# Kernel tuning notes

Measured on AMD Instinct MI355X. Metric: run time of the kernel, lower is better.

Reference implementation:

```python
import jax, jax.numpy as jnp
import numpy as np

N_QUBITS = 20
W_MUL = (2.0 ** 0.5) * (5.0 ** -0.5)  # he_std = gain * 5**-0.5, use_wscale=True, lrmul=1

_C = jnp.complex64
X = jnp.array([[0, 1], [1, 0]], dtype=_C)
Y = jnp.array([[0, -1j], [1j, 0]], dtype=_C)
Z = jnp.array([[1, 0], [0, -1]], dtype=_C)
I2 = jnp.eye(2, dtype=_C)
I4 = jnp.eye(4, dtype=_C)
XX = jnp.kron(X, X)
YY = jnp.kron(Y, Y)
ZZ = jnp.kron(Z, Z)


def _rot(theta, pauli, ident):
    # exp(-i * theta/2 * P) = cos(theta/2) I - i sin(theta/2) P
    a = theta * 0.5
    return jnp.cos(a) * ident - (1j * jnp.sin(a)) * pauli


def _apply_1q(state, g, w):
    # state: [batch] + [2]*n ; contract gate input index with qubit axis w
    s = jnp.tensordot(g, state, axes=((1,), (w + 1,)))
    return jnp.moveaxis(s, 0, w + 1)


def _apply_2q(state, g4, w0, w1):
    g = g4.reshape(2, 2, 2, 2)  # (out0, out1, in0, in1)
    s = jnp.tensordot(g, state, axes=((2, 3), (w0 + 1, w1 + 1)))
    return jnp.moveaxis(s, (0, 1), (w0 + 1, w1 + 1))


def _xyz_layer(psi, params, n):
    # params: [3n]; rx, ry, rz on each wire
    for q in range(n):
        psi = _apply_1q(psi, _rot(params[3 * q], X, I2), q)
        psi = _apply_1q(psi, _rot(params[3 * q + 1], Y, I2), q)
        psi = _apply_1q(psi, _rot(params[3 * q + 2], Z, I2), q)
    return psi


def _circuit(psi, w, n):
    psi = _xyz_layer(psi, w[: 3 * n], n)
    for q in range(n - 1):
        i = 3 * n + 3 * q
        psi = _apply_2q(psi, _rot(w[i], XX, I4), q, q + 1)
        psi = _apply_2q(psi, _rot(w[i + 1], YY, I4), q, q + 1)
        psi = _apply_2q(psi, _rot(w[i + 2], ZZ, I4), q, q + 1)
    psi = _xyz_layer(psi, w[6 * n - 3 :], n)
    return psi


def setup_inputs() -> dict:
    key = jax.random.key(0)
    k1, k2 = jax.random.split(key)
    n = N_QUBITS
    dim = 1 << n
    batch = 4
    x = jax.random.normal(k1, (batch, 1, dim), dtype=jnp.float32)
    weight = jax.random.uniform(k2, (9 * n - 3,), dtype=jnp.float32, minval=0.0, maxval=2.0 * np.pi)
    return {"x": x, "weight": weight, "dimA": 10}


def reference(x, weight, dimA):
    n = N_QUBITS
    batch = x.shape[0]
    w = weight * W_MUL
    psi = x.astype(_C).reshape((batch,) + (2,) * n)  # MPS tensor [b, 2, ..., 2]
    psi = _circuit(psi, w, n)
    dimB = n - dimA
    # partial trace of |psi><psi| over the first dimB qubits (most-significant axes):
    # reduced[a, c] = sum_t psi[t, a] * conj(psi[t, c])  -- never materialize the full DM
    psi = psi.reshape(batch, 1 << dimB, 1 << dimA)
    rdm = jnp.einsum('bta,btc->bac', psi, psi.conj())
    # return real/imag stacked on last axis (real-valued representation of complex DM)
    return jnp.stack([rdm.real, rdm.imag], axis=-1)
```

## Files before the change

### kernel.cpp

```cpp
#include <hip/hip_runtime.h>
#include <hip/hip_bf16.h>

#define N_Q    20
#define DIM    (1 << N_Q)
#define BATCH  4
#define NGATES 19
#define L2OFF  117

typedef float2 c32;
typedef __attribute__((ext_vector_type(8))) short short8;
typedef __attribute__((ext_vector_type(4))) float f32x4;

__device__ __forceinline__ c32 cmul(c32 a, c32 b) {
    return make_float2(fmaf(a.x, b.x, -a.y * b.y), fmaf(a.x, b.y, a.y * b.x));
}
__device__ __forceinline__ c32 cmadd(c32 acc, c32 a, c32 b) {
    acc.x = fmaf(a.x, b.x, fmaf(-a.y, b.y, acc.x));
    acc.y = fmaf(a.x, b.y, fmaf(a.y, b.x, acc.y));
    return acc;
}
__device__ __forceinline__ unsigned short f2bf(float f) {
    union { float f; unsigned u; } v; v.f = f;
    unsigned r = v.u + 0x7FFFu + ((v.u >> 16) & 1u);
    return (unsigned short)(r >> 16);
}

__device__ void mm2(const c32 A[2][2], const c32 B[2][2], c32 C[2][2]) {
    for (int i = 0; i < 2; i++)
        for (int j = 0; j < 2; j++) {
            c32 s = make_float2(0.f, 0.f);
            for (int k = 0; k < 2; k++) s = cmadd(s, A[i][k], B[k][j]);
            C[i][j] = s;
        }
}
__device__ void mm4(const c32 A[4][4], const c32 B[4][4], c32 C[4][4]) {
    for (int i = 0; i < 4; i++)
        for (int j = 0; j < 4; j++) {
            c32 s = make_float2(0.f, 0.f);
            for (int k = 0; k < 4; k++) s = cmadd(s, A[i][k], B[k][j]);
            C[i][j] = s;
        }
}
__device__ void single_u(const float* w, int base, c32 U[2][2]) {
    const float WM = 0.63245553203367586640f;
    float hx = w[base] * WM * 0.5f, hy = w[base + 1] * WM * 0.5f, hz = w[base + 2] * WM * 0.5f;
    float cx = cosf(hx), sx = sinf(hx);
    float cy = cosf(hy), sy = sinf(hy);
    float cz = cosf(hz), sz = sinf(hz);
    c32 RX[2][2] = {{{cx, 0.f}, {0.f, -sx}}, {{0.f, -sx}, {cx, 0.f}}};
    c32 RY[2][2] = {{{cy, 0.f}, {-sy, 0.f}}, {{sy, 0.f}, {cy, 0.f}}};
    c32 RZ[2][2] = {{{cz, -sz}, {0.f, 0.f}}, {{0.f, 0.f}, {cz, sz}}};
    c32 T[2][2];
    mm2(RY, RX, T);
    mm2(RZ, T, U);
}
__device__ void kron22(const c32 A[2][2], const c32 B[2][2], c32 K[4][4]) {
    for (int i = 0; i < 2; i++)
        for (int j = 0; j < 2; j++)
            for (int k = 0; k < 2; k++)
                for (int l = 0; l < 2; l++)
                    K[i * 2 + j][k * 2 + l] = cmul(A[i][k], B[j][l]);
}

__global__ void build_gates(const float* __restrict__ w, c32* __restrict__ G) {
    int q = threadIdx.x;
    if (q >= NGATES) return;
    const float WM = 0.63245553203367586640f;
    float hx = w[60 + 3 * q] * WM * 0.5f;
    float hy = w[61 + 3 * q] * WM * 0.5f;
    float hz = w[62 + 3 * q] * WM * 0.5f;
    float cx = cosf(hx), sx = sinf(hx);
    float cy = cosf(hy), sy = sinf(hy);
    float cz = cosf(hz), sz = sinf(hz);
    c32 RXX[4][4], RYY[4][4], RZZ[4][4];
    for (int i = 0; i < 4; i++)
        for (int j = 0; j < 4; j++) {
            RXX[i][j] = make_float2(0.f, 0.f);
            RYY[i][j] = make_float2(0.f, 0.f);
            RZZ[i][j] = make_float2(0.f, 0.f);
        }
    for (int i = 0; i < 4; i++) {
        RXX[i][i]     = make_float2(cx, 0.f);
        RXX[i][3 - i] = make_float2(0.f, -sx);
        RYY[i][i]     = make_float2(cy, 0.f);
    }
    RYY[0][3] = make_float2(0.f,  sy);
    RYY[1][2] = make_float2(0.f, -sy);
    RYY[2][1] = make_float2(0.f, -sy);
    RYY[3][0] = make_float2(0.f,  sy);
    RZZ[0][0] = make_float2(cz, -sz);
    RZZ[1][1] = make_float2(cz,  sz);
    RZZ[2][2] = make_float2(cz,  sz);
    RZZ[3][3] = make_float2(cz, -sz);
    c32 T[4][4], M[4][4];
    mm4(RYY, RXX, T);
    mm4(RZZ, T, M);

    c32 I2m[2][2] = {{{1.f, 0.f}, {0.f, 0.f}}, {{0.f, 0.f}, {1.f, 0.f}}};
    c32 Ua[2][2], Ub[2][2], Pre[4][4], Post[4][4];
    if (q == 0) {
        single_u(w, 0, Ua);
        single_u(w, 3, Ub);
        kron22(Ua, Ub, Pre);
    } else {
        single_u(w, 3 * (q + 1), Ub);
        kron22(I2m, Ub, Pre);
    }
    if (q == NGATES - 1) {
        single_u(w, L2OFF + 3 * 18, Ua);
        single_u(w, L2OFF + 3 * 19, Ub);
        kron22(Ua, Ub, Post);
    } else {
        single_u(w, L2OFF + 3 * q, Ua);
        kron22(Ua, I2m, Post);
    }
    c32 T2[4][4], Gq[4][4];
    mm4(M, Pre, T2);
    mm4(Post, T2, Gq);
    for (int i = 0; i < 4; i++)
        for (int j = 0; j < 4; j++)
            G[q * 16 + i * 4 + j] = Gq[i][j];
}

__device__ __forceinline__ void apply4(const c32* g, c32& x0, c32& x1, c32& x2, c32& x3) {
    c32 r0 = cmul(g[0],  x0); r0 = cmadd(r0, g[1],  x1); r0 = cmadd(r0, g[2],  x2); r0 = cmadd(r0, g[3],  x3);
    c32 r1 = cmul(g[4],  x0); r1 = cmadd(r1, g[5],  x1); r1 = cmadd(r1, g[6],  x2); r1 = cmadd(r1, g[7],  x3);
    c32 r2 = cmul(g[8],  x0); r2 = cmadd(r2, g[9],  x1); r2 = cmadd(r2, g[10], x2); r2 = cmadd(r2, g[11], x3);
    c32 r3 = cmul(g[12], x0); r3 = cmadd(r3, g[13], x1); r3 = cmadd(r3, g[14], x2); r3 = cmadd(r3, g[15], x3);
    x0 = r0; x1 = r1; x2 = r2; x3 = r3;
}
__device__ __forceinline__ void load_gate(const c32* __restrict__ gp, c32 g[16]) {
#pragma unroll
    for (int k = 0; k < 16; k++) g[k] = gp[k];
}
template <int LO>
__device__ __forceinline__ void gate_on32(c32 v[32], const c32 g[16]) {
#pragma unroll
    for (int m = 0; m < 8; ++m) {
        const int j0 = ((m >> LO) << (LO + 2)) | (m & ((1 << LO) - 1));
        const int s = 1 << LO;
        apply4(g, v[j0], v[j0 + s], v[j0 + 2 * s], v[j0 + 3 * s]);
    }
}
template <int LO>
__device__ __forceinline__ void gate_on16(c32* v, const c32 g[16]) {
#pragma unroll
    for (int m = 0; m < 4; ++m) {
        const int j0 = ((m >> LO) << (LO + 2)) | (m & ((1 << LO) - 1));
        const int s = 1 << LO;
        apply4(g, v[j0], v[j0 + s], v[j0 + 2 * s], v[j0 + 3 * s]);
    }
}

#define SIDX(l) ((l) ^ ((((l) >> 5) & 15)))

__global__ __launch_bounds__(256) void pass_a2(const float* __restrict__ x,
                                               c32* __restrict__ psi,
                                               const c32* __restrict__ Gall) {
    __shared__ c32 s[8192];
    int b = blockIdx.x >> 7;
    int c0 = (blockIdx.x & 127) << 5;
    const float* xp = x + ((size_t)b << 20) + c0;
    c32* pp = psi + ((size_t)b << 20) + c0;
    int t = threadIdx.x;
    int col = t & 31, rlow = t >> 5;
    c32 v[32], g[16];
#pragma unroll
    for (int j = 0; j < 32; ++j) {
        int row = (j << 3) | rlow;
        v[j] = make_float2(xp[(size_t)row * 4096 + col], 0.f);
    }
    load_gate(Gall + 0 * 16, g);  gate_on32<3>(v, g);
    load_gate(Gall + 1 * 16, g);  gate_on32<2>(v, g);
    load_gate(Gall + 2 * 16, g);  gate_on32<1>(v, g);
    load_gate(Gall + 3 * 16, g);  gate_on32<0>(v, g);
#pragma unroll
    for (int j = 0; j < 32; ++j) {
        int l = ((((j << 3) | rlow) << 5)) | col;
        s[SIDX(l)] = v[j];
    }
    __syncthreads();
    int rhi = t >> 5;
#pragma unroll
    for (int rtop = 0; rtop < 2; ++rtop)
#pragma unroll
        for (int j = 0; j < 16; ++j) {
            int row = (rtop << 7) | (rhi << 4) | j;
            int l = (row << 5) | col;
            v[rtop * 16 + j] = s[SIDX(l)];
        }
    load_gate(Gall + 4 * 16, g);  gate_on16<2>(v, g);  gate_on16<2>(v + 16, g);
    load_gate(Gall + 5 * 16, g);  gate_on16<1>(v, g);  gate_on16<1>(v + 16, g);
    load_gate(Gall + 6 * 16, g);  gate_on16<0>(v, g);  gate_on16<0>(v + 16, g);
#pragma unroll
    for (int rtop = 0; rtop < 2; ++rtop)
#pragma unroll
        for (int j = 0; j < 16; ++j) {
            int row = (rtop << 7) | (rhi << 4) | j;
            pp[(size_t)row * 4096 + col] = v[rtop * 16 + j];
        }
}

__global__ __launch_bounds__(256) void pass_b2(const c32* __restrict__ psi,
                                               unsigned short* __restrict__ Brt,
                                               unsigned short* __restrict__ Bit,
                                               const c32* __restrict__ Gall) {
    __shared__ c32 s[8192];
    int b = blockIdx.x >> 7;
    int chunk = blockIdx.x & 127;
    const c32* pp = psi + ((size_t)b << 20) + ((size_t)chunk << 13);
    int t = threadIdx.x;
    c32 v[32], g[16];
#pragma unroll
    for (int j = 0; j < 32; ++j) v[j] = pp[(j << 8) | t];
    load_gate(Gall + 7 * 16, g);   gate_on32<3>(v, g);
    load_gate(Gall + 8 * 16, g);   gate_on32<2>(v, g);
    load_gate(Gall + 9 * 16, g);   gate_on32<1>(v, g);
    load_gate(Gall + 10 * 16, g);  gate_on32<0>(v, g);
#pragma unroll
    for (int j = 0; j < 32; ++j) { int l = (j << 8) | t; s[SIDX(l)] = v[j]; }
    __syncthreads();
    int hi2 = (t >> 4) << 9, lo2 = t & 15;
#pragma unroll
    for (int j = 0; j < 32; ++j) { int l = hi2 | (j << 4) | lo2; v[j] = s[SIDX(l)]; }
    load_gate(Gall + 11 * 16, g);  gate_on32<3>(v, g);
    load_gate(Gall + 12 * 16, g);  gate_on32<2>(v, g);
    load_gate(Gall + 13 * 16, g);  gate_on32<1>(v, g);
    load_gate(Gall + 14 * 16, g);  gate_on32<0>(v, g);
    __syncthreads();
#pragma unroll
    for (int j = 0; j < 32; ++j) { int l = hi2 | (j << 4) | lo2; s[SIDX(l)] = v[j]; }
    __syncthreads();
#pragma unroll
    for (int j = 0; j < 32; ++j) { int l = (t << 5) | j; v[j] = s[SIDX(l)]; }
    load_gate(Gall + 15 * 16, g);  gate_on32<3>(v, g);
    load_gate(Gall + 16 * 16, g);  gate_on32<2>(v, g);
    load_gate(Gall + 17 * 16, g);  gate_on32<1>(v, g);
    load_gate(Gall + 18 * 16, g);  gate_on32<0>(v, g);
    size_t off = ((size_t)b << 20) + ((size_t)chunk << 13) + ((size_t)t << 5);
#pragma unroll
    for (int p = 0; p < 4; ++p) {
        unsigned short rr[8], ri[8];
#pragma unroll
        for (int i = 0; i < 8; ++i) {
            rr[i] = f2bf(v[8 * p + i].x);
            ri[i] = f2bf(v[8 * p + i].y);
        }
        *reinterpret_cast<float4*>(Brt + off + 8 * p) = *reinterpret_cast<float4*>(rr);
        *reinterpret_cast<float4*>(Bit + off + 8 * p) = *reinterpret_cast<float4*>(ri);
    }
}

__global__ __launch_bounds__(256) void bt_t(const unsigned short* __restrict__ Brt,
                                            const unsigned short* __restrict__ Bit,
                                            unsigned short* __restrict__ Art,
                                            unsigned short* __restrict__ Ait) {
    __shared__ unsigned lds32[64 * 66];
    int b  = blockIdx.z;
    int t0 = blockIdx.x * 64;
    int a0 = blockIdx.y * 64;
    size_t gb = (size_t)b << 20;
#pragma unroll
    for (int h = 0; h < 2; ++h) {
        int p = threadIdx.x + h * 256;
        int r = p >> 3, cq = p & 7;
        size_t src = gb + (size_t)(t0 + r) * 1024 + a0 + cq * 8;
        float4 fr = *reinterpret_cast<const float4*>(Brt + src);
        float4 fi = *reinterpret_cast<const float4*>(Bit + src);
        const unsigned short* ur = reinterpret_cast<const unsigned short*>(&fr);
        const unsigned short* ui = reinterpret_cast<const unsigned short*>(&fi);
#pragma unroll
        for (int i = 0; i < 8; ++i)
            lds32[r * 66 + cq * 8 + i] = (unsigned)ur[i] | ((unsigned)ui[i] << 16);
    }
    __syncthreads();
#pragma unroll
    for (int h = 0; h < 2; ++h) {
        int q = threadIdx.x + h * 256;
        int a = q >> 3, tq = q & 7;
        unsigned short rr[8], ri[8];
#pragma unroll
        for (int i = 0; i < 8; ++i) {
            unsigned w = lds32[(tq * 8 + i) * 66 + a];
            rr[i] = (unsigned short)(w & 0xFFFF);
            ri[i] = (unsigned short)(w >> 16);
        }
        size_t dst = gb + (size_t)(a0 + a) * 1024 + t0 + tq * 8;
        *reinterpret_cast<float4*>(Art + dst) = *reinterpret_cast<float4*>(rr);
        *reinterpret_cast<float4*>(Ait + dst) = *reinterpret_cast<float4*>(ri);
    }
}

#define LDP 72
__global__ __launch_bounds__(256) void gram_mfma(const unsigned short* __restrict__ Art,
                                                 const unsigned short* __restrict__ Ait,
                                                 float2* __restrict__ out) {
    __shared__ unsigned short ldsRr[64 * LDP], ldsRi[64 * LDP];
    __shared__ unsigned short ldsCr[64 * LDP], ldsCi[64 * LDP];
    int b = blockIdx.y;
    int rem = blockIdx.x;
    int ia = 0;
    while (rem >= 16 - ia) { rem -= 16 - ia; ++ia; }
    int ic = ia + rem;
    int a0 = ia * 64, c0 = ic * 64;

    int lane = threadIdx.x & 63;
    int w = threadIdx.x >> 6;
    int wr = (w >> 1) * 32, wc = (w & 1) * 32;
    int lrow = lane & 15;
    int lk   = (lane >> 4) * 8;

    f32x4 accS[2][2], accP1[2][2], accP2[2][2];
#pragma unroll
    for (int m = 0; m < 2; m++)
#pragma unroll
        for (int n = 0; n < 2; n++) {
            accS[m][n] = (f32x4)0.f; accP1[m][n] = (f32x4)0.f; accP2[m][n] = (f32x4)0.f;
        }

    size_t gb = (size_t)b << 20;
    for (int k0 = 0; k0 < 1024; k0 += 64) {
        __syncthreads();
#pragma unroll
        for (int s = 0; s < 2; ++s) {
            int cchunk = threadIdx.x + s * 256;
            int row = cchunk >> 3;
            int col = (cchunk & 7) * 8;
            size_t gR = gb + ((size_t)(a0 + row) << 10) + k0 + col;
            size_t gC = gb + ((size_t)(c0 + row) << 10) + k0 + col;
            float4 vRr = *reinterpret_cast<const float4*>(Art + gR);
            float4 vRi = *reinterpret_cast<const float4*>(Ait + gR);
            float4 vCr = *reinterpret_cast<const float4*>(Art + gC);
            float4 vCi = *reinterpret_cast<const float4*>(Ait + gC);
            int la = row * LDP + col;
            *reinterpret_cast<float4*>(ldsRr + la) = vRr;
            *reinterpret_cast<float4*>(ldsRi + la) = vRi;
            *reinterpret_cast<float4*>(ldsCr + la) = vCr;
            *reinterpret_cast<float4*>(ldsCi + la) = vCi;
        }
        __syncthreads();
#pragma unroll
        for (int kk = 0; kk < 2; ++kk) {
            int ko = kk * 32 + lk;
            short8 ar[2], ai[2], br[2], bi[2];
#pragma unroll
            for (int m = 0; m < 2; m++) {
                int r = (wr + m * 16 + lrow) * LDP + ko;
                ar[m] = *reinterpret_cast<const short8*>(ldsRr + r);
                ai[m] = *reinterpret_cast<const short8*>(ldsRi + r);
            }
#pragma unroll
            for (int n = 0; n < 2; n++) {
                int r = (wc + n * 16 + lrow) * LDP + ko;
                br[n] = *reinterpret_cast<const short8*>(ldsCr + r);
                bi[n] = *reinterpret_cast<const short8*>(ldsCi + r);
            }
#pragma unroll
            for (int m = 0; m < 2; m++)
#pragma unroll
                for (int n = 0; n < 2; n++) {
                    accS[m][n]  = __builtin_amdgcn_mfma_f32_16x16x32_bf16(ar[m], br[n], accS[m][n], 0, 0, 0);
                    accS[m][n]  = __builtin_amdgcn_mfma_f32_16x16x32_bf16(ai[m], bi[n], accS[m][n], 0, 0, 0);
                    accP1[m][n] = __builtin_amdgcn_mfma_f32_16x16x32_bf16(ai[m], br[n], accP1[m][n], 0, 0, 0);
                    accP2[m][n] = __builtin_amdgcn_mfma_f32_16x16x32_bf16(ar[m], bi[n], accP2[m][n], 0, 0, 0);
                }
        }
    }
    size_t ob = (size_t)b << 20;
#pragma unroll
    for (int m = 0; m < 2; m++)
#pragma unroll
        for (int n = 0; n < 2; n++)
#pragma unroll
            for (int r = 0; r < 4; r++) {
                int a = a0 + wr + m * 16 + (lane >> 4) * 4 + r;
                int c = c0 + wc + n * 16 + (lane & 15);
                float re = accS[m][n][r];
                float im = accP1[m][n][r] - accP2[m][n][r];
                out[ob + ((size_t)a << 10) + c] = make_float2(re, im);
                if (ia != ic)
                    out[ob + ((size_t)c << 10) + a] = make_float2(re, -im);
            }
}

extern "C" void kernel_launch(void* const* d_in, const int* in_sizes, int n_in,
                              void* d_out, int out_size, void* d_ws, size_t ws_size,
                              hipStream_t stream) {
    const float* x = (const float*)d_in[0];
    const float* weight = (const float*)d_in[1];
    const size_t psiBytes = (size_t)BATCH * DIM * sizeof(c32);
    const size_t planeBytes = (size_t)BATCH * DIM * sizeof(unsigned short);
    c32* psi = (c32*)d_ws;
    c32* G = (c32*)((char*)d_ws + psiBytes);
    unsigned short* Brt = (unsigned short*)((char*)d_ws + psiBytes + 65536);
    unsigned short* Bit = Brt + (size_t)BATCH * DIM;
    unsigned short* Art = Bit + (size_t)BATCH * DIM;
    unsigned short* Ait = Art + (size_t)BATCH * DIM;

    build_gates<<<1, 64, 0, stream>>>(weight, G);
    pass_a2<<<BATCH * 128, 256, 0, stream>>>(x, psi, G);
    pass_b2<<<BATCH * 128, 256, 0, stream>>>(psi, Brt, Bit, G);
    bt_t<<<dim3(16, 16, BATCH), 256, 0, stream>>>(Brt, Bit, Art, Ait);
    gram_mfma<<<dim3(136, BATCH), 256, 0, stream>>>(Art, Ait, (float2*)d_out);
}
```

Measured before the change: 105.9 us.

## Double-buffer gram panels via direct global-to-LDS loads and stage input through LDS

```diff
diff --git a/kernel.cpp b/kernel.cpp
--- a/kernel.cpp
+++ b/kernel.cpp
@@ -10,6 +10,7 @@
 typedef float2 c32;
 typedef __attribute__((ext_vector_type(8))) short short8;
 typedef __attribute__((ext_vector_type(4))) float f32x4;
+typedef __attribute__((ext_vector_type(4))) unsigned int u32x4;
 
 __device__ __forceinline__ c32 cmul(c32 a, c32 b) {
     return make_float2(fmaf(a.x, b.x, -a.y * b.y), fmaf(a.x, b.y, a.y * b.x));
@@ -23,6 +24,10 @@
     union { float f; unsigned u; } v; v.f = f;
     unsigned r = v.u + 0x7FFFu + ((v.u >> 16) & 1u);
     return (unsigned short)(r >> 16);
+}
+__device__ __forceinline__ void gll16(const void* g, void* l) {
+    __builtin_amdgcn_global_load_lds((const __attribute__((address_space(1))) void*)g,
+                                     (__attribute__((address_space(3))) void*)l, 16, 0, 0);
 }
 
 __device__ void mm2(const c32 A[2][2], const c32 B[2][2], c32 C[2][2]) {
@@ -157,19 +162,31 @@
 __global__ __launch_bounds__(256) void pass_a2(const float* __restrict__ x,
                                                c32* __restrict__ psi,
                                                const c32* __restrict__ Gall) {
-    __shared__ c32 s[8192];
+    __shared__ __align__(16) char smem[65536];
+    float* xs = (float*)smem;
+    c32* s = (c32*)smem;
     int b = blockIdx.x >> 7;
     int c0 = (blockIdx.x & 127) << 5;
     const float* xp = x + ((size_t)b << 20) + c0;
     c32* pp = psi + ((size_t)b << 20) + c0;
     int t = threadIdx.x;
+#pragma unroll
+    for (int i = 0; i < 8; ++i) {
+        int f4 = t + (i << 8);
+        int row = f4 >> 3, sl = f4 & 7;
+        float4 v = *reinterpret_cast<const float4*>(xp + (size_t)row * 4096 + sl * 4);
+        reinterpret_cast<float4*>(xs)[row * 8 + (sl ^ (row & 7))] = v;
+    }
+    __syncthreads();
     int col = t & 31, rlow = t >> 5;
     c32 v[32], g[16];
 #pragma unroll
     for (int j = 0; j < 32; ++j) {
         int row = (j << 3) | rlow;
-        v[j] = make_float2(xp[(size_t)row * 4096 + col], 0.f);
-    }
+        float re = xs[row * 32 + ((((col >> 2) ^ (row & 7)) << 2) | (col & 3))];
+        v[j] = make_float2(re, 0.f);
+    }
+    __syncthreads();
     load_gate(Gall + 0 * 16, g);  gate_on32<3>(v, g);
     load_gate(Gall + 1 * 16, g);  gate_on32<2>(v, g);
     load_gate(Gall + 2 * 16, g);  gate_on32<1>(v, g);
@@ -291,80 +308,76 @@
     }
 }
 
-#define LDP 72
-__global__ __launch_bounds__(256) void gram_mfma(const unsigned short* __restrict__ Art,
-                                                 const unsigned short* __restrict__ Ait,
-                                                 float2* __restrict__ out) {
-    __shared__ unsigned short ldsRr[64 * LDP], ldsRi[64 * LDP];
-    __shared__ unsigned short ldsCr[64 * LDP], ldsCi[64 * LDP];
+__device__ __forceinline__ void stage_panel(const unsigned short* __restrict__ sp, size_t gb,
+                                            int prow, int kt, unsigned short* dst, int lane) {
+    int srow = lane >> 3, sslot = lane & 7;
+#pragma unroll
+    for (int i = 0; i < 8; ++i) {
+        int r = (i << 3) | srow;
+        int sl = sslot ^ srow;
+        const unsigned short* gp = sp + gb + ((size_t)(prow + r) << 10) + kt * 64 + sl * 8;
+        gll16(gp, dst + i * 512);
+    }
+}
+__global__ __launch_bounds__(256) void gram_mfma2(const unsigned short* __restrict__ Art,
+                                                  const unsigned short* __restrict__ Ait,
+                                                  float2* __restrict__ out) {
+    __shared__ unsigned short lds[2][4][4096];
     int b = blockIdx.y;
     int rem = blockIdx.x;
     int ia = 0;
     while (rem >= 16 - ia) { rem -= 16 - ia; ++ia; }
     int ic = ia + rem;
     int a0 = ia * 64, c0 = ic * 64;
-
-    int lane = threadIdx.x & 63;
-    int w = threadIdx.x >> 6;
+    int lane = threadIdx.x & 63, w = threadIdx.x >> 6;
     int wr = (w >> 1) * 32, wc = (w & 1) * 32;
-    int lrow = lane & 15;
-    int lk   = (lane >> 4) * 8;
-
-    f32x4 accS[2][2], accP1[2][2], accP2[2][2];
+    const unsigned short* sp = (w & 1) ? Ait : Art;
+    int prow = (w < 2) ? a0 : c0;
+    size_t gb = (size_t)b << 20;
+
+    f32x4 accRe[2][2], accIm[2][2];
 #pragma unroll
     for (int m = 0; m < 2; m++)
 #pragma unroll
-        for (int n = 0; n < 2; n++) {
-            accS[m][n] = (f32x4)0.f; accP1[m][n] = (f32x4)0.f; accP2[m][n] = (f32x4)0.f;
-        }
-
-    size_t gb = (size_t)b << 20;
-    for (int k0 = 0; k0 < 1024; k0 += 64) {
+        for (int n = 0; n < 2; n++) { accRe[m][n] = (f32x4)0.f; accIm[m][n] = (f32x4)0.f; }
+
+    stage_panel(sp, gb, prow, 0, &lds[0][w][0], lane);
+    __syncthreads();
+    for (int kt = 0; kt < 16; ++kt) {
+        int cur = kt & 1;
+        if (kt < 15) stage_panel(sp, gb, prow, kt + 1, &lds[cur ^ 1][w][0], lane);
+#pragma unroll
+        for (int kk = 0; kk < 2; ++kk) {
+            int sbase = kk * 4 + (lane >> 4);
+            short8 ar[2], ai[2], br[2], bi[2];
+#pragma unroll
+            for (int m = 0; m < 2; m++) {
+                int r = wr + m * 16 + (lane & 15);
+                int off = r * 64 + ((sbase ^ (r & 7)) << 3);
+                ar[m] = *reinterpret_cast<const short8*>(&lds[cur][0][off]);
+                ai[m] = *reinterpret_cast<const short8*>(&lds[cur][1][off]);
+            }
+#pragma unroll
+            for (int n = 0; n < 2; n++) {
+                int r = wc + n * 16 + (lane & 15);
+                int off = r * 64 + ((sbase ^ (r & 7)) << 3);
+                br[n] = *reinterpret_cast<const short8*>(&lds[cur][2][off]);
+                bi[n] = *reinterpret_cast<const short8*>(&lds[cur][3][off]);
+            }
+#pragma unroll
+            for (int m = 0; m < 2; m++) {
+                u32x4 tn = *reinterpret_cast<u32x4*>(&ar[m]) ^ 0x80008000u;
+                short8 arn = *reinterpret_cast<short8*>(&tn);
+#pragma unroll
+                for (int n = 0; n < 2; n++) {
+                    accRe[m][n] = __builtin_amdgcn_mfma_f32_16x16x32_bf16(ar[m],  br[n], accRe[m][n], 0, 0, 0);
+                    accRe[m][n] = __builtin_amdgcn_mfma_f32_16x16x32_bf16(ai[m],  bi[n], accRe[m][n], 0, 0, 0);
+                    accIm[m][n] = __builtin_amdgcn_mfma_f32_16x16x32_bf16(ai[m],  br[n], accIm[m][n], 0, 0, 0);
+                    accIm[m][n] = __builtin_amdgcn_mfma_f32_16x16x32_bf16(arn,    bi[n], accIm[m][n], 0, 0, 0);
+                }
+            }
+        }
         __syncthreads();
-#pragma unroll
-        for (int s = 0; s < 2; ++s) {
-            int cchunk = threadIdx.x + s * 256;
-            int row = cchunk >> 3;
-            int col = (cchunk & 7) * 8;
-            size_t gR = gb + ((size_t)(a0 + row) << 10) + k0 + col;
-            size_t gC = gb + ((size_t)(c0 + row) << 10) + k0 + col;
-            float4 vRr = *reinterpret_cast<const float4*>(Art + gR);
-            float4 vRi = *reinterpret_cast<const float4*>(Ait + gR);
-            float4 vCr = *reinterpret_cast<const float4*>(Art + gC);
-            float4 vCi = *reinterpret_cast<const float4*>(Ait + gC);
-            int la = row * LDP + col;
-            *reinterpret_cast<float4*>(ldsRr + la) = vRr;
-            *reinterpret_cast<float4*>(ldsRi + la) = vRi;
-            *reinterpret_cast<float4*>(ldsCr + la) = vCr;
-            *reinterpret_cast<float4*>(ldsCi + la) = vCi;
-        }
-        __syncthreads();
-#pragma unroll
-        for (int kk = 0; kk < 2; ++kk) {
-            int ko = kk * 32 + lk;
-            short8 ar[2], ai[2], br[2], bi[2];
-#pragma unroll
-            for (int m = 0; m < 2; m++) {
-                int r = (wr + m * 16 + lrow) * LDP + ko;
-                ar[m] = *reinterpret_cast<const short8*>(ldsRr + r);
-                ai[m] = *reinterpret_cast<const short8*>(ldsRi + r);
-            }
-#pragma unroll
-            for (int n = 0; n < 2; n++) {
-                int r = (wc + n * 16 + lrow) * LDP + ko;
-                br[n] = *reinterpret_cast<const short8*>(ldsCr + r);
-                bi[n] = *reinterpret_cast<const short8*>(ldsCi + r);
-            }
-#pragma unroll
-            for (int m = 0; m < 2; m++)
-#pragma unroll
-                for (int n = 0; n < 2; n++) {
-                    accS[m][n]  = __builtin_amdgcn_mfma_f32_16x16x32_bf16(ar[m], br[n], accS[m][n], 0, 0, 0);
-                    accS[m][n]  = __builtin_amdgcn_mfma_f32_16x16x32_bf16(ai[m], bi[n], accS[m][n], 0, 0, 0);
-                    accP1[m][n] = __builtin_amdgcn_mfma_f32_16x16x32_bf16(ai[m], br[n], accP1[m][n], 0, 0, 0);
-                    accP2[m][n] = __builtin_amdgcn_mfma_f32_16x16x32_bf16(ar[m], bi[n], accP2[m][n], 0, 0, 0);
-                }
-        }
     }
     size_t ob = (size_t)b << 20;
 #pragma unroll
@@ -375,8 +388,8 @@
             for (int r = 0; r < 4; r++) {
                 int a = a0 + wr + m * 16 + (lane >> 4) * 4 + r;
                 int c = c0 + wc + n * 16 + (lane & 15);
-                float re = accS[m][n][r];
-                float im = accP1[m][n][r] - accP2[m][n][r];
+                float re = accRe[m][n][r];
+                float im = accIm[m][n][r];
                 out[ob + ((size_t)a << 10) + c] = make_float2(re, im);
                 if (ia != ic)
                     out[ob + ((size_t)c << 10) + a] = make_float2(re, -im);
@@ -389,7 +402,6 @@
     const float* x = (const float*)d_in[0];
     const float* weight = (const float*)d_in[1];
     const size_t psiBytes = (size_t)BATCH * DIM * sizeof(c32);
-    const size_t planeBytes = (size_t)BATCH * DIM * sizeof(unsigned short);
     c32* psi = (c32*)d_ws;
     c32* G = (c32*)((char*)d_ws + psiBytes);
     unsigned short* Brt = (unsigned short*)((char*)d_ws + psiBytes + 65536);
@@ -401,5 +413,5 @@
     pass_a2<<<BATCH * 128, 256, 0, stream>>>(x, psi, G);
     pass_b2<<<BATCH * 128, 256, 0, stream>>>(psi, Brt, Bit, G);
     bt_t<<<dim3(16, 16, BATCH), 256, 0, stream>>>(Brt, Bit, Art, Ait);
-    gram_mfma<<<dim3(136, BATCH), 256, 0, stream>>>(Art, Ait, (float2*)d_out);
-}
+    gram_mfma2<<<dim3(136, BATCH), 256, 0, stream>>>(Art, Ait, (float2*)d_out);
+}
```

Measured after the change: 106.7 us. About the same (+0.7%).
